# Optimization experiments

Hardware: AMD Instinct MI355X
Metric: run time of the kernel (lower is better)

## Reference

```python
import jax, jax.numpy as jnp
import numpy as np

NUM_HEADS = 8


def setup_inputs() -> dict:
    key = jax.random.key(0)
    ks = jax.random.split(key, 7)
    B, D, N = 16, 512, 2048
    sc = 1.0 / np.sqrt(D)
    return {
        "X_Query": jax.random.normal(ks[0], (B, D, N), jnp.float32),
        "X_Key": jax.random.normal(ks[1], (B, D, N), jnp.float32),
        "X_Value": jax.random.normal(ks[2], (B, D, N), jnp.float32),
        "W_q": jax.random.normal(ks[3], (D, D), jnp.float32) * sc,
        "W_k": jax.random.normal(ks[4], (D, D), jnp.float32) * sc,
        "W_v": jax.random.normal(ks[5], (D, D), jnp.float32) * sc,
        "W_o": jax.random.normal(ks[6], (D, D), jnp.float32) * sc,
    }


def _proj(W, x):
    # Conv1d(D, D, kernel_size=1, bias=False) == channel matmul
    return jnp.einsum('oi,bin->bon', W, x)


def _split_heads(x, h):
    # torch: cat(x.chunk(h, dim=-1), dim=0) -> (h, B, D, N/h) stacked layout
    B, D, N = x.shape
    return x.reshape(B, D, h, N // h).transpose(2, 0, 1, 3)


def _mha(XQ, XK, XV, Wq, Wk, Wv, Wo):
    B, D, N = XQ.shape
    h = NUM_HEADS
    Nh = N // h
    q = _split_heads(_proj(Wq, XQ), h)  # (h, B, D, Nh)
    k = _split_heads(_proj(Wk, XK), h)
    v = _split_heads(_proj(Wv, XV), h)
    # scores over the CHANNEL axis: (h, B, D, D), scaled by sqrt(d_k)=sqrt(Nh)
    scores = jnp.einsum('hbdn,hben->hbde', q, k) / jnp.sqrt(jnp.asarray(Nh, q.dtype))
    p = jax.nn.softmax(scores, axis=-1)
    out = jnp.einsum('hbde,hben->hbdn', p, v)  # (h, B, D, Nh)
    # torch: cat(chunks, dim=0) inverse -> cat along dim=-1
    attn_heads = out.transpose(1, 2, 0, 3).reshape(B, D, N)
    return _proj(Wo, XQ - attn_heads)


def reference(X_Query, X_Key, X_Value, W_q, W_k, W_v, W_o):
    return _mha(X_Query, X_Key, X_Value, W_q, W_k, W_v, W_o)
```

## Files before the change

### kernel.cpp

```cpp
#include <hip/hip_runtime.h>
#include <hip/hip_bf16.h>

#define DD  512
#define NN  2048
#define BB  16
#define NHD 256

typedef unsigned short u16;
typedef __attribute__((ext_vector_type(4))) float f32x4;
typedef __attribute__((ext_vector_type(8))) short s16x8;
typedef __attribute__((ext_vector_type(4))) short s16x4;
typedef __attribute__((ext_vector_type(4))) u16   u16x4;

static __device__ __forceinline__ u16 f2bf(float f) {
  __hip_bfloat16 h = __float2bfloat16(f);
  return *reinterpret_cast<u16*>(&h);
}
static __device__ __forceinline__ float bf2f(u16 u) {
  union { unsigned int i; float f; } v; v.i = ((unsigned int)u) << 16; return v.f;
}
static __device__ __forceinline__ f32x4 mfma_bf16(s16x8 a, s16x8 b, f32x4 c) {
  return __builtin_amdgcn_mfma_f32_16x16x32_bf16(a, b, c, 0, 0, 0);
}
static __device__ __forceinline__ void gload_lds16(const u16* g, u16* l) {
  __builtin_amdgcn_global_load_lds(
      (const __attribute__((address_space(1))) unsigned int*)g,
      (__attribute__((address_space(3))) unsigned int*)l, 16, 0, 0);
}
static __device__ __forceinline__ void barrier_raw() {
  __builtin_amdgcn_sched_barrier(0);
  __builtin_amdgcn_s_barrier();
  __builtin_amdgcn_sched_barrier(0);
}
#define WAITCNT(s) do { asm volatile("s_waitcnt " s ::: "memory"); \
                        __builtin_amdgcn_sched_barrier(0); } while (0)

__global__ __launch_bounds__(256) void k_cvt_w(const float* __restrict__ w0,
                                               const float* __restrict__ w1,
                                               const float* __restrict__ w2,
                                               const float* __restrict__ w3,
                                               u16* __restrict__ out) {
  const float* srcs[4] = {w0, w1, w2, w3};
  const float* s = srcs[blockIdx.y];
  u16* o = out + (size_t)blockIdx.y * (DD * DD);
  int idx = blockIdx.x * 256 + threadIdx.x;
  float4 v = *(const float4*)(s + (size_t)idx * 4);
  u16x4 u = {f2bf(v.x), f2bf(v.y), f2bf(v.z), f2bf(v.w)};
  *(u16x4*)(o + (size_t)idx * 4) = u;
}

__global__ __launch_bounds__(256) void k_transpose3(const float* __restrict__ x0,
                                                    const float* __restrict__ x1,
                                                    const float* __restrict__ x2,
                                                    u16* __restrict__ o0,
                                                    u16* __restrict__ o1,
                                                    u16* __restrict__ o2) {
  __shared__ float t[64][65];
  const int tid = threadIdx.x;
  const int z = blockIdx.z, which = z >> 4, b = z & 15;
  const float* X = which == 0 ? x0 : (which == 1 ? x1 : x2);
  u16*       XT = which == 0 ? o0 : (which == 1 ? o1 : o2);
  const int n0 = blockIdx.x * 64, d0 = blockIdx.y * 64;
  const float* Xb = X + ((size_t)b * DD + d0) * NN + n0;
#pragma unroll
  for (int i = 0; i < 4; ++i) {
    int r = (tid >> 4) + i * 16;
    int c = (tid & 15) * 4;
    float4 v = *(const float4*)(Xb + (size_t)r * NN + c);
    t[r][c] = v.x; t[r][c + 1] = v.y; t[r][c + 2] = v.z; t[r][c + 3] = v.w;
  }
  __syncthreads();
  u16* Ob = XT + ((size_t)b * NN + n0) * DD + d0;
#pragma unroll
  for (int i = 0; i < 4; ++i) {
    int n = (tid >> 4) + i * 16;
    int d = (tid & 15) * 4;
    u16x4 u = {f2bf(t[d][n]), f2bf(t[d + 1][n]), f2bf(t[d + 2][n]), f2bf(t[d + 3][n])};
    *(u16x4*)(Ob + (size_t)n * DD + d) = u;
  }
}

#define GEMM_STAGE(Ag, lda, Bg, ldb, buf, kt)                                   \
  {                                                                             \
    _Pragma("unroll")                                                           \
    for (int j = 0; j < 4; ++j) {                                               \
      int s = j * 256 + w * 64 + lane;                                          \
      int row = s >> 3, u = s & 7;                                              \
      int col = ((u ^ (row & 7)) * 8);                                          \
      gload_lds16(Ag + (size_t)row * lda + (kt) * 64 + col, &Ab[buf][s * 8]);   \
      gload_lds16(Bg + (size_t)row * ldb + (kt) * 64 + col, &Bb[buf][s * 8]);   \
    }                                                                           \
  }

#define GEMM_COMPUTE(buf)                                                       \
  {                                                                             \
    _Pragma("unroll")                                                           \
    for (int ks = 0; ks < 2; ++ks) {                                            \
      s16x8 av[4], bv[4];                                                       \
      _Pragma("unroll")                                                         \
      for (int m = 0; m < 4; ++m) {                                             \
        int row = wm + m * 16 + r;                                              \
        av[m] = *(const s16x8*)&Ab[buf][row * 64 + (((ks * 4 + g) ^ (row & 7)) * 8)]; \
      }                                                                         \
      _Pragma("unroll")                                                         \
      for (int nf = 0; nf < 4; ++nf) {                                          \
        int row = wn + nf * 16 + r;                                             \
        bv[nf] = *(const s16x8*)&Bb[buf][row * 64 + (((ks * 4 + g) ^ (row & 7)) * 8)]; \
      }                                                                         \
      _Pragma("unroll")                                                         \
      for (int m = 0; m < 4; ++m)                                               \
        _Pragma("unroll")                                                       \
        for (int nf = 0; nf < 4; ++nf)                                          \
          acc[m][nf] = mfma_bf16(av[m], bv[nf], acc[m][nf]);                    \
    }                                                                           \
  }

#define GEMM_PREAMBLE                                                           \
  __shared__ __align__(16) u16 Ab[2][128 * 64];                                 \
  __shared__ __align__(16) u16 Bb[2][128 * 64];                                 \
  const int tid = threadIdx.x;                                                  \
  const int lane = tid & 63, w = tid >> 6;                                      \
  const int wm = (w >> 1) * 64, wn = (w & 1) * 64;                              \
  const int r = lane & 15, g = lane >> 4;                                       \
  f32x4 acc[4][4] = {};

#define GEMM_MAINLOOP(Ag, lda, Bg, ldb, nkt)                                    \
  GEMM_STAGE(Ag, lda, Bg, ldb, 0, 0);                                           \
  __syncthreads();                                                              \
  for (int kt = 0; kt < (nkt) - 1; ++kt) {                                      \
    GEMM_STAGE(Ag, lda, Bg, ldb, (kt & 1) ^ 1, kt + 1);                         \
    GEMM_COMPUTE(kt & 1);                                                       \
    __syncthreads();                                                            \
  }                                                                             \
  GEMM_COMPUTE(((nkt) - 1) & 1);

template <typename OUT_T>
__global__ __launch_bounds__(256) void k_gemm_nt(
    const u16* __restrict__ A, long long a_bs, int lda,
    const u16* __restrict__ B, long long b_bs, int ldb,
    OUT_T* __restrict__ C, long long c_bs, int ldc, int K) {
  GEMM_PREAMBLE
  const int m0 = blockIdx.x * 128, n0 = blockIdx.y * 128;
  const u16* Ag = A + (size_t)blockIdx.z * a_bs + (size_t)m0 * lda;
  const u16* Bg = B + (size_t)blockIdx.z * b_bs + (size_t)n0 * ldb;
  const int nkt = K >> 6;
  GEMM_MAINLOOP(Ag, lda, Bg, ldb, nkt);

  OUT_T* Cg = C + (size_t)blockIdx.z * c_bs;
#pragma unroll
  for (int m = 0; m < 4; ++m)
#pragma unroll
    for (int nf = 0; nf < 4; ++nf)
#pragma unroll
      for (int j = 0; j < 4; ++j) {
        int row = m0 + wm + m * 16 + g * 4 + j;
        int col = n0 + wn + nf * 16 + r;
        float v = acc[m][nf][j];
        if constexpr (sizeof(OUT_T) == 2) Cg[(size_t)row * ldc + col] = f2bf(v);
        else                              Cg[(size_t)row * ldc + col] = v;
      }
}

__global__ __launch_bounds__(512, 4) void k_attn_fused(
    const u16* __restrict__ Qdn, const u16* __restrict__ Kdn,
    const u16* __restrict__ VT,  const u16* __restrict__ XqT,
    u16* __restrict__ And) {
  __shared__ __align__(16) u16 L[35072];
  u16* Kr = L;
  u16* Vr = L + 16384;
  u16* Ps = L + 32768;

  const int tid = threadIdx.x;
  const int lane = tid & 63, w = tid >> 6;
  const int r = lane & 15, g = lane >> 4;
  const int dq = w >> 1, eh = w & 1;
  const int nq = w >> 1, dh = w & 1;
  const int bid = blockIdx.x;
  const int dt = bid >> 7, hb = bid & 127;
  const int h = hb & 7, b = hb >> 3;
  const int d0 = dt * 64, hn0 = h * NHD;

  const u16* Qg = Qdn + ((size_t)b * DD + d0) * NN + hn0;
  const u16* Kg = Kdn + ((size_t)b * DD) * NN + hn0;
  const u16* Vg = VT + ((size_t)b * NN + hn0) * DD;

  auto stage_ket = [&](int et) {
    u16* dst = Kr + (et & 1) * 8192;
    const u16* src = Kg + (size_t)(et * 32) * NN;
#pragma unroll
    for (int j = 0; j < 2; ++j) {
      int s = j * 512 + tid;
      int row = s >> 5, u = s & 31;
      gload_lds16(src + (size_t)row * NN + ((u ^ (row & 7)) * 8), dst + s * 8);
    }
  };
  auto stage_vet = [&](int et) {
    u16* dst = Vr + (et & 1) * 8192;
    int rl = tid >> 2, u = tid & 3;
#pragma unroll
    for (int j = 0; j < 2; ++j) {
      int gn = (rl >> 5) * 64 + j * 32 + (rl & 31);
      gload_lds16(Vg + (size_t)gn * DD + et * 32 + ((u ^ (rl & 3)) * 8),
                  dst + j * 4096 + tid * 8);
    }
  };

#pragma unroll
  for (int jj = 0; jj < 4; ++jj) {
    int s = jj * 512 + tid;
    int row = s >> 5, u = s & 31;
    gload_lds16(Qg + (size_t)row * NN + ((u ^ (row & 7)) * 8), L + s * 8);
  }
  WAITCNT("vmcnt(0)");
  barrier_raw();
  s16x8 qf[8];
  {
    const int qrow = dq * 16 + r;
#pragma unroll
    for (int k2 = 0; k2 < 8; ++k2)
      qf[k2] = *(const s16x8*)&L[qrow * 256 + (((k2 * 4 + g) ^ (qrow & 7)) * 8)];
  }
  WAITCNT("lgkmcnt(0)");
  barrier_raw();
  stage_ket(0); stage_vet(0);

  float psum[4] = {};
  f32x4 acc_o[2][2][2] = {};

#pragma unroll
  for (int et = 0; et < 16; ++et) {
    WAITCNT("vmcnt(2)");
    barrier_raw();
    f32x4 acc_s = {};
    const u16* kb = Kr + (et & 1) * 8192;
    const int rowe = eh * 16 + r;
    __builtin_amdgcn_s_setprio(1);
#pragma unroll
    for (int kq = 0; kq < 8; ++kq) {
      s16x8 bv = *(const s16x8*)&kb[rowe * 256 + (((kq * 4 + g) ^ (rowe & 7)) * 8)];
      acc_s = mfma_bf16(qf[kq], bv, acc_s);
    }
    __builtin_amdgcn_s_setprio(0);
    WAITCNT("lgkmcnt(0)");
    barrier_raw();
    if (et + 1 < 16) { stage_ket(et + 1); stage_vet(et + 1); }
#pragma unroll
    for (int j = 0; j < 4; ++j) {
      int rowd = dq * 16 + g * 4 + j;
      int cole = eh * 16 + r;
      float p = __expf(acc_s[j] * 0.0625f);
      psum[j] += p;
      Ps[rowd * 36 + cole] = f2bf(p);
    }
    WAITCNT("lgkmcnt(0)");
    if (et < 15) WAITCNT("vmcnt(4)");
    else         WAITCNT("vmcnt(0)");
    barrier_raw();
    s16x8 pb[2];
#pragma unroll
    for (int nf = 0; nf < 2; ++nf) {
      int rowd = dh * 32 + nf * 16 + r;
      s16x4 plo = *(const s16x4*)&Ps[rowd * 36 + g * 8];
      s16x4 phi = *(const s16x4*)&Ps[rowd * 36 + g * 8 + 4];
      pb[nf] = __builtin_shufflevector(plo, phi, 0, 1, 2, 3, 4, 5, 6, 7);
    }
    __builtin_amdgcn_s_setprio(1);
#pragma unroll
    for (int j = 0; j < 2; ++j) {
      const u16* vb = Vr + (et & 1) * 8192 + j * 4096;
#pragma unroll
      for (int ms = 0; ms < 2; ++ms) {
        int rl = nq * 32 + ms * 16 + r;
        s16x8 av = *(const s16x8*)((const char*)vb + rl * 64 + ((g * 16) ^ ((rl & 3) << 4)));
        acc_o[j][ms][0] = mfma_bf16(av, pb[0], acc_o[j][ms][0]);
        acc_o[j][ms][1] = mfma_bf16(av, pb[1], acc_o[j][ms][1]);
      }
    }
    __builtin_amdgcn_s_setprio(0);
    WAITCNT("lgkmcnt(0)");
  }

  barrier_raw();
  float* rs = (float*)L;
#pragma unroll
  for (int j = 0; j < 4; ++j) {
    float v = psum[j];
    v += __shfl_xor(v, 1);
    v += __shfl_xor(v, 2);
    v += __shfl_xor(v, 4);
    v += __shfl_xor(v, 8);
    if (r == 0) rs[w * 16 + g * 4 + j] = v;
  }
  __syncthreads();
  if (tid < 64) {
    int dqi = tid >> 4, i = tid & 15;
    rs[128 + tid] = 1.0f / (rs[(dqi * 2) * 16 + i] + rs[(dqi * 2 + 1) * 16 + i]);
  }
  __syncthreads();

  const u16* Xg = XqT + ((size_t)b * NN + hn0) * DD + d0;
  u16* Ag = And + ((size_t)b * NN + hn0) * DD + d0;
#pragma unroll
  for (int j = 0; j < 2; ++j)
#pragma unroll
    for (int ms = 0; ms < 2; ++ms)
#pragma unroll
      for (int nf = 0; nf < 2; ++nf) {
        const int dc = dh * 32 + nf * 16 + r;
        const float inv = rs[128 + dc];
#pragma unroll
        for (int jj = 0; jj < 4; ++jj) {
          const int npos = nq * 64 + j * 32 + ms * 16 + g * 4 + jj;
          float o = acc_o[j][ms][nf][jj] * inv;
          float xq = bf2f(Xg[(size_t)npos * DD + dc]);
          Ag[(size_t)npos * DD + dc] = f2bf(xq - o);
        }
      }
}

extern "C" void kernel_launch(void* const* d_in, const int* in_sizes, int n_in,
                              void* d_out, int out_size, void* d_ws, size_t ws_size,
                              hipStream_t stream) {
  const float* Xq = (const float*)d_in[0];
  const float* Xk = (const float*)d_in[1];
  const float* Xv = (const float*)d_in[2];
  const float* Wq = (const float*)d_in[3];
  const float* Wk = (const float*)d_in[4];
  const float* Wv = (const float*)d_in[5];
  const float* Wo = (const float*)d_in[6];
  float* out = (float*)d_out;

  char* ws = (char*)d_ws;
  const size_t MB = 1024 * 1024;
  u16* Wb  = (u16*)ws;
  u16* XqT = (u16*)(ws + 2 * MB);
  u16* XvT = (u16*)(ws + 34 * MB);
  u16* And = XvT;
  u16* Qdn = (u16*)(ws + 66 * MB);
  u16* XkT = (u16*)(ws + 98 * MB);
  u16* VTb = (u16*)d_out;
  u16* Kdn = (u16*)d_out + (size_t)BB * NN * DD;

  k_cvt_w<<<dim3(256, 4), 256, 0, stream>>>(Wq, Wk, Wv, Wo, Wb);

  k_transpose3<<<dim3(NN / 64, DD / 64, BB * 3), 256, 0, stream>>>(
      Xq, Xk, Xv, XqT, XkT, XvT);

  k_gemm_nt<u16><<<dim3(NN / 128, DD / 128, BB), 256, 0, stream>>>(
      XvT, (long long)NN * DD, DD,
      Wb + 2 * DD * DD, 0, DD,
      VTb, (long long)NN * DD, DD, DD);
  k_gemm_nt<u16><<<dim3(DD / 128, NN / 128, BB), 256, 0, stream>>>(
      Wb, 0, DD,
      XqT, (long long)NN * DD, DD,
      Qdn, (long long)DD * NN, NN, DD);
  k_gemm_nt<u16><<<dim3(DD / 128, NN / 128, BB), 256, 0, stream>>>(
      Wb + 1 * DD * DD, 0, DD,
      XkT, (long long)NN * DD, DD,
      Kdn, (long long)DD * NN, NN, DD);

  k_attn_fused<<<dim3(1024), 512, 0, stream>>>(Qdn, Kdn, VTb, XqT, And);

  k_gemm_nt<float><<<dim3(DD / 128, NN / 128, BB), 256, 0, stream>>>(
      Wb + 3 * DD * DD, 0, DD,
      And, (long long)NN * DD, DD,
      out, (long long)DD * NN, NN, DD);
}
```

Baseline: 267.1 us.

## Fuse input transpose and bf16 conversion into projection GEMM loads

Removes the separate transpose kernel that wrote bf16 transposed copies of Xq, Xk and Xv. The projection GEMMs now read fp32 X directly into registers, convert to bf16 and transpose while writing to LDS, and the attention epilogue reads the fp32 Xq residual directly. This saves a full read and write pass over three large activation tensors, but the register-staged X load is synchronous (vmcnt(0) each k-step). It also drops unrolling of the attention et-loop, which may change scheduling.

```diff
diff --git a/kernel.cpp b/kernel.cpp
--- a/kernel.cpp
+++ b/kernel.cpp
@@ -49,35 +49,108 @@
   *(u16x4*)(o + (size_t)idx * 4) = u;
 }
 
-__global__ __launch_bounds__(256) void k_transpose3(const float* __restrict__ x0,
-                                                    const float* __restrict__ x1,
-                                                    const float* __restrict__ x2,
-                                                    u16* __restrict__ o0,
-                                                    u16* __restrict__ o1,
-                                                    u16* __restrict__ o2) {
-  __shared__ float t[64][65];
+template <bool XA>
+__global__ __launch_bounds__(256) void k_gemm_proj(
+    const float* __restrict__ X, const u16* __restrict__ W,
+    u16* __restrict__ C, long long c_bs, int ldc) {
+  __shared__ __align__(16) u16 Xb[2][128 * 64];
+  __shared__ __align__(16) u16 Wt[2][128 * 64];
   const int tid = threadIdx.x;
-  const int z = blockIdx.z, which = z >> 4, b = z & 15;
-  const float* X = which == 0 ? x0 : (which == 1 ? x1 : x2);
-  u16*       XT = which == 0 ? o0 : (which == 1 ? o1 : o2);
-  const int n0 = blockIdx.x * 64, d0 = blockIdx.y * 64;
-  const float* Xb = X + ((size_t)b * DD + d0) * NN + n0;
-#pragma unroll
-  for (int i = 0; i < 4; ++i) {
-    int r = (tid >> 4) + i * 16;
-    int c = (tid & 15) * 4;
-    float4 v = *(const float4*)(Xb + (size_t)r * NN + c);
-    t[r][c] = v.x; t[r][c + 1] = v.y; t[r][c + 2] = v.z; t[r][c + 3] = v.w;
-  }
-  __syncthreads();
-  u16* Ob = XT + ((size_t)b * NN + n0) * DD + d0;
-#pragma unroll
-  for (int i = 0; i < 4; ++i) {
-    int n = (tid >> 4) + i * 16;
-    int d = (tid & 15) * 4;
-    u16x4 u = {f2bf(t[d][n]), f2bf(t[d + 1][n]), f2bf(t[d + 2][n]), f2bf(t[d + 3][n])};
-    *(u16x4*)(Ob + (size_t)n * DD + d) = u;
-  }
+  const int lane = tid & 63, w = tid >> 6;
+  const int wm = (w >> 1) * 64, wn = (w & 1) * 64;
+  const int r = lane & 15, g = lane >> 4;
+  f32x4 acc[4][4] = {};
+
+  const int m0 = blockIdx.x * 128, n0 = blockIdx.y * 128, b = blockIdx.z;
+  const int xbase = XA ? m0 : n0;
+  const int wbase = XA ? n0 : m0;
+  const float* Xg = X + (size_t)b * DD * NN + xbase;
+  const u16* Wg = W + (size_t)wbase * DD;
+
+  const int nq = tid & 31, ib = (tid >> 5) * 4;
+  float4 rv[8];
+  auto issue_x = [&](int kt) {
+#pragma unroll
+    for (int j = 0; j < 2; ++j)
+#pragma unroll
+      for (int ii = 0; ii < 4; ++ii)
+        rv[j * 4 + ii] =
+            *(const float4*)(Xg + (size_t)(kt * 64 + j * 32 + ib + ii) * NN + nq * 4);
+  };
+  auto stage_w = [&](int buf, int kt) {
+#pragma unroll
+    for (int j2 = 0; j2 < 4; ++j2) {
+      int s = j2 * 256 + tid;
+      int row = s >> 3, u = s & 7;
+      gload_lds16(Wg + (size_t)row * DD + kt * 64 + ((u ^ (row & 7)) * 8),
+                  &Wt[buf][s * 8]);
+    }
+  };
+  auto write_x = [&](int buf) {
+#pragma unroll
+    for (int j = 0; j < 2; ++j) {
+      const int k0 = j * 32 + ib;
+      const float4 a0 = rv[j*4], a1 = rv[j*4+1], a2 = rv[j*4+2], a3 = rv[j*4+3];
+#pragma unroll
+      for (int e = 0; e < 4; ++e) {
+        const int row = nq * 4 + e;
+        float v0, v1, v2, v3;
+        if      (e == 0) { v0=a0.x; v1=a1.x; v2=a2.x; v3=a3.x; }
+        else if (e == 1) { v0=a0.y; v1=a1.y; v2=a2.y; v3=a3.y; }
+        else if (e == 2) { v0=a0.z; v1=a1.z; v2=a2.z; v3=a3.z; }
+        else             { v0=a0.w; v1=a1.w; v2=a2.w; v3=a3.w; }
+        u16x4 pk = {f2bf(v0), f2bf(v1), f2bf(v2), f2bf(v3)};
+        *(u16x4*)((char*)&Xb[buf][0] + row * 128 +
+                  (((k0 >> 3) ^ (row & 7)) * 16) + (k0 & 7) * 2) = pk;
+      }
+    }
+  };
+
+  issue_x(0); stage_w(0, 0);
+  for (int kt = 0; kt < 8; ++kt) {
+    WAITCNT("vmcnt(0)");
+    barrier_raw();
+    write_x(kt & 1);
+    if (kt < 7) { issue_x(kt + 1); stage_w((kt + 1) & 1, kt + 1); }
+    WAITCNT("lgkmcnt(0)");
+    barrier_raw();
+    {
+      const u16* Ab_ = XA ? &Xb[kt & 1][0] : &Wt[kt & 1][0];
+      const u16* Bb_ = XA ? &Wt[kt & 1][0] : &Xb[kt & 1][0];
+#pragma unroll
+      for (int ks = 0; ks < 2; ++ks) {
+        s16x8 av[4], bv[4];
+#pragma unroll
+        for (int m = 0; m < 4; ++m) {
+          int row = wm + m * 16 + r;
+          av[m] = *(const s16x8*)&Ab_[row * 64 + (((ks * 4 + g) ^ (row & 7)) * 8)];
+        }
+#pragma unroll
+        for (int nf = 0; nf < 4; ++nf) {
+          int row = wn + nf * 16 + r;
+          bv[nf] = *(const s16x8*)&Bb_[row * 64 + (((ks * 4 + g) ^ (row & 7)) * 8)];
+        }
+#pragma unroll
+        for (int m = 0; m < 4; ++m)
+#pragma unroll
+          for (int nf = 0; nf < 4; ++nf)
+            acc[m][nf] = mfma_bf16(av[m], bv[nf], acc[m][nf]);
+      }
+    }
+    WAITCNT("lgkmcnt(0)");
+  }
+
+  u16* Cg = C + (size_t)b * c_bs;
+#pragma unroll
+  for (int m = 0; m < 4; ++m)
+#pragma unroll
+    for (int nf = 0; nf < 4; ++nf)
+#pragma unroll
+      for (int j = 0; j < 4; ++j) {
+        int row = m0 + wm + m * 16 + g * 4 + j;
+        int col = n0 + wn + nf * 16 + r;
+        Cg[(size_t)row * ldc + col] = f2bf(acc[m][nf][j]);
+      }
 }
 
 #define GEMM_STAGE(Ag, lda, Bg, ldb, buf, kt)                                   \
@@ -163,7 +236,7 @@
 
 __global__ __launch_bounds__(512, 4) void k_attn_fused(
     const u16* __restrict__ Qdn, const u16* __restrict__ Kdn,
-    const u16* __restrict__ VT,  const u16* __restrict__ XqT,
+    const u16* __restrict__ VT,  const float* __restrict__ Xq,
     u16* __restrict__ And) {
   __shared__ __align__(16) u16 L[35072];
   u16* Kr = L;
@@ -227,7 +300,6 @@
   float psum[4] = {};
   f32x4 acc_o[2][2][2] = {};
 
-#pragma unroll
   for (int et = 0; et < 16; ++et) {
     WAITCNT("vmcnt(2)");
     barrier_raw();
@@ -298,7 +370,7 @@
   }
   __syncthreads();
 
-  const u16* Xg = XqT + ((size_t)b * NN + hn0) * DD + d0;
+  const float* Xqf = Xq + ((size_t)b * DD + d0) * NN + hn0;
   u16* Ag = And + ((size_t)b * NN + hn0) * DD + d0;
 #pragma unroll
   for (int j = 0; j < 2; ++j)
@@ -312,7 +384,7 @@
         for (int jj = 0; jj < 4; ++jj) {
           const int npos = nq * 64 + j * 32 + ms * 16 + g * 4 + jj;
           float o = acc_o[j][ms][nf][jj] * inv;
-          float xq = bf2f(Xg[(size_t)npos * DD + dc]);
+          float xq = Xqf[(size_t)dc * NN + npos];
           Ag[(size_t)npos * DD + dc] = f2bf(xq - o);
         }
       }
@@ -333,33 +405,21 @@
   char* ws = (char*)d_ws;
   const size_t MB = 1024 * 1024;
   u16* Wb  = (u16*)ws;
-  u16* XqT = (u16*)(ws + 2 * MB);
-  u16* XvT = (u16*)(ws + 34 * MB);
-  u16* And = XvT;
-  u16* Qdn = (u16*)(ws + 66 * MB);
-  u16* XkT = (u16*)(ws + 98 * MB);
+  u16* Qdn = (u16*)(ws + 2 * MB);
+  u16* And = (u16*)(ws + 34 * MB);
   u16* VTb = (u16*)d_out;
   u16* Kdn = (u16*)d_out + (size_t)BB * NN * DD;
 
   k_cvt_w<<<dim3(256, 4), 256, 0, stream>>>(Wq, Wk, Wv, Wo, Wb);
 
-  k_transpose3<<<dim3(NN / 64, DD / 64, BB * 3), 256, 0, stream>>>(
-      Xq, Xk, Xv, XqT, XkT, XvT);
-
-  k_gemm_nt<u16><<<dim3(NN / 128, DD / 128, BB), 256, 0, stream>>>(
-      XvT, (long long)NN * DD, DD,
-      Wb + 2 * DD * DD, 0, DD,
-      VTb, (long long)NN * DD, DD, DD);
-  k_gemm_nt<u16><<<dim3(DD / 128, NN / 128, BB), 256, 0, stream>>>(
-      Wb, 0, DD,
-      XqT, (long long)NN * DD, DD,
-      Qdn, (long long)DD * NN, NN, DD);
-  k_gemm_nt<u16><<<dim3(DD / 128, NN / 128, BB), 256, 0, stream>>>(
-      Wb + 1 * DD * DD, 0, DD,
-      XkT, (long long)NN * DD, DD,
-      Kdn, (long long)DD * NN, NN, DD);
-
-  k_attn_fused<<<dim3(1024), 512, 0, stream>>>(Qdn, Kdn, VTb, XqT, And);
+  k_gemm_proj<false><<<dim3(DD / 128, NN / 128, BB), 256, 0, stream>>>(
+      Xq, Wb, Qdn, (long long)DD * NN, NN);
+  k_gemm_proj<false><<<dim3(DD / 128, NN / 128, BB), 256, 0, stream>>>(
+      Xk, Wb + DD * DD, Kdn, (long long)DD * NN, NN);
+  k_gemm_proj<true><<<dim3(NN / 128, DD / 128, BB), 256, 0, stream>>>(
+      Xv, Wb + 2 * DD * DD, VTb, (long long)NN * DD, DD);
+
+  k_attn_fused<<<dim3(1024), 512, 0, stream>>>(Qdn, Kdn, VTb, Xq, And);
 
   k_gemm_nt<float><<<dim3(DD / 128, NN / 128, BB), 256, 0, stream>>>(
       Wb + 3 * DD * DD, 0, DD,
```

New measurement: 256.5 us. -4.0%, faster.
